# Kernel tuning notes

Hardware: AMD Instinct MI355X
Metric: run time of the kernel (lower is better)

Reference implementation:

```python
import jax, jax.numpy as jnp
import numpy as np

B, S, H, NH, PF, L, V = 8, 1024, 1024, 16, 4096, 6, 32000
HD = H // NH
STD = 0.02
NEG = -1e10


def setup_inputs() -> dict:
    key = jax.random.key(0)
    ks = jax.random.split(key, 12)
    inp = {
        "src": jax.random.randint(ks[0], (B, S), 0, V),
        "src_mask": jnp.ones((B, 1, 1, S), dtype=bool),
        "tok_emb": jax.random.normal(ks[1], (V, H), jnp.float32) * STD,
        "pos_emb": jax.random.normal(ks[2], (S, H), jnp.float32) * STD,
        "Wq": jax.random.normal(ks[3], (L, H, H), jnp.float32) * STD,
        "bq": jnp.zeros((L, H), jnp.float32),
        "Wk": jax.random.normal(ks[4], (L, H, H), jnp.float32) * STD,
        "bk": jnp.zeros((L, H), jnp.float32),
        "Wv": jax.random.normal(ks[5], (L, H, H), jnp.float32) * STD,
        "bv": jnp.zeros((L, H), jnp.float32),
        "Wo": jax.random.normal(ks[6], (L, H, H), jnp.float32) * STD,
        "bo": jnp.zeros((L, H), jnp.float32),
        "W1": jax.random.normal(ks[7], (L, H, PF), jnp.float32) * STD,
        "b1": jnp.zeros((L, PF), jnp.float32),
        "W2": jax.random.normal(ks[8], (L, PF, H), jnp.float32) * STD,
        "b2": jnp.zeros((L, H), jnp.float32),
        "ln1_g": jnp.ones((L, H), jnp.float32),
        "ln1_b": jnp.zeros((L, H), jnp.float32),
        "ln2_g": jnp.ones((L, H), jnp.float32),
        "ln2_b": jnp.zeros((L, H), jnp.float32),
    }
    return inp


def layer_norm(x, g, b, eps=1e-5):
    m = jnp.mean(x, axis=-1, keepdims=True)
    v = jnp.mean((x - m) ** 2, axis=-1, keepdims=True)
    return (x - m) * jax.lax.rsqrt(v + eps) * g + b


def reference(src, src_mask, tok_emb, pos_emb, Wq, bq, Wk, bk, Wv, bv, Wo, bo,
              W1, b1, W2, b2, ln1_g, ln1_b, ln2_g, ln2_b):
    # embedding * sqrt(hid_dim) + positional embedding (dropout = identity at eval)
    x = tok_emb[src] * jnp.sqrt(jnp.float32(H)) + pos_emb[None, :S]
    attn_scale = jnp.sqrt(jnp.float32(HD))
    for l in range(L):
        # multi-head self-attention
        q = (x @ Wq[l] + bq[l]).reshape(B, S, NH, HD).transpose(0, 2, 1, 3)
        k = (x @ Wk[l] + bk[l]).reshape(B, S, NH, HD).transpose(0, 2, 1, 3)
        v = (x @ Wv[l] + bv[l]).reshape(B, S, NH, HD).transpose(0, 2, 1, 3)
        energy = jnp.einsum('bhqd,bhkd->bhqk', q, k) / attn_scale  # [B,NH,S,S]
        energy = jnp.where(src_mask, energy, NEG)
        attn = jax.nn.softmax(energy, axis=-1)
        o = jnp.einsum('bhqk,bhkd->bhqd', attn, v)
        o = o.transpose(0, 2, 1, 3).reshape(B, S, H) @ Wo[l] + bo[l]
        x = layer_norm(x + o, ln1_g[l], ln1_b[l])
        # position-wise feedforward
        f = jax.nn.relu(x @ W1[l] + b1[l]) @ W2[l] + b2[l]
        x = layer_norm(x + f, ln2_g[l], ln2_b[l])
    return x
```

## Files before the change

### kernel.cpp

```cpp
#include <hip/hip_runtime.h>
#include <cstdint>
#include <cstddef>


#define DI __device__ __forceinline__

typedef __attribute__((ext_vector_type(8))) short short8;
typedef __attribute__((ext_vector_type(4))) short s16x4;
typedef __attribute__((ext_vector_type(4))) float f32x4;
typedef __attribute__((ext_vector_type(4))) unsigned u32x4;

static constexpr int H  = 1024;
static constexpr int S  = 1024;
static constexpr int BB = 8;
static constexpr int NH = 16;
static constexpr int PF = 4096;
static constexpr int M  = BB * S;
static constexpr int L  = 6;

DI short f2bf(float f) {
  unsigned u = __builtin_bit_cast(unsigned, f);
  u += 0x7fffu + ((u >> 16) & 1u);
  return (short)(u >> 16);
}

DI unsigned packbf(float a, float b) {
  return (__builtin_bit_cast(unsigned, a) >> 16) |
         (__builtin_bit_cast(unsigned, b) & 0xffff0000u);
}

DI void async16(void* lds, const void* g) {
  __builtin_amdgcn_global_load_lds(
      (const __attribute__((address_space(1))) unsigned*)g,
      (__attribute__((address_space(3))) unsigned*)lds, 16, 0, 0);
}

DI f32x4 mfma16(short8 a, short8 b, f32x4 c) {
  return __builtin_amdgcn_mfma_f32_16x16x32_bf16(a, b, c, 0, 0, 0);
}

__global__ __launch_bounds__(256) void embed_kernel(
    const int* __restrict__ src, const float* __restrict__ tok,
    const float* __restrict__ pos, float* __restrict__ xf,
    short* __restrict__ xb) {
  const int row = blockIdx.x;
  const int s = row & (S - 1);
  const int i0 = threadIdx.x << 2;
  const int v = src[row];
  const float4 te = *(const float4*)(tok + (size_t)v * H + i0);
  const float4 pe = *(const float4*)(pos + (size_t)s * H + i0);
  float o[4] = {te.x * 32.f + pe.x, te.y * 32.f + pe.y,
                te.z * 32.f + pe.z, te.w * 32.f + pe.w};
  *(float4*)(xf + (size_t)row * H + i0) = make_float4(o[0], o[1], o[2], o[3]);
  s16x4 pk;
  pk[0] = f2bf(o[0]); pk[1] = f2bf(o[1]); pk[2] = f2bf(o[2]); pk[3] = f2bf(o[3]);
  *(s16x4*)(xb + (size_t)row * H + i0) = pk;
}

__global__ __launch_bounds__(256) void wconv_layer(
    const float* __restrict__ Wq, const float* __restrict__ Wk,
    const float* __restrict__ Wv, const float* __restrict__ Wo,
    const float* __restrict__ W1, const float* __restrict__ W2,
    const float* __restrict__ bq, const float* __restrict__ bk,
    const float* __restrict__ bv, short* __restrict__ tq,
    short* __restrict__ tk, short* __restrict__ tv, short* __restrict__ to,
    short* __restrict__ t1, short* __restrict__ t2, float* __restrict__ bqkv) {
  const int id = blockIdx.x;
  if (id >= 3072) {
    const int i = (id - 3072) * 256 + threadIdx.x;
    bqkv[i] = (i < 1024) ? bq[i] : (i < 2048) ? bk[i - 1024] : bv[i - 2048];
    return;
  }
  const float* W; short* Wt; int K, N, lb;
  if (id < 256)       { W = Wq; Wt = tq; K = 1024; N = 1024; lb = id; }
  else if (id < 512)  { W = Wk; Wt = tk; K = 1024; N = 1024; lb = id - 256; }
  else if (id < 768)  { W = Wv; Wt = tv; K = 1024; N = 1024; lb = id - 512; }
  else if (id < 1024) { W = Wo; Wt = to; K = 1024; N = 1024; lb = id - 768; }
  else if (id < 2048) { W = W1; Wt = t1; K = 1024; N = 4096; lb = id - 1024; }
  else                { W = W2; Wt = t2; K = 4096; N = 1024; lb = id - 2048; }
  __shared__ float tile[64][65];
  const int ntn = N >> 6;
  const int k0 = (lb / ntn) << 6;
  const int n0 = (lb % ntn) << 6;
  const int r4 = threadIdx.x >> 6, cc = threadIdx.x & 63;
#pragma unroll
  for (int i = 0; i < 16; i++) {
    const int r = (i << 2) + r4;
    tile[r][cc] = W[(size_t)(k0 + r) * N + n0 + cc];
  }
  __syncthreads();
#pragma unroll
  for (int i = 0; i < 16; i++) {
    const int n = (i << 2) + r4;
    Wt[(size_t)(n0 + n) * K + k0 + cc] = f2bf(tile[cc][n]);
  }
}

template <int EPI>
__global__ __launch_bounds__(512, 2) void gemmT(
    const short* __restrict__ A, const short* __restrict__ Bt,
    const float* __restrict__ bias, void* __restrict__ out0,
    short* __restrict__ outK, short* __restrict__ outV,
    const int nbn, const int outN, const int K) {
  extern __shared__ char lds[];
  constexpr int BUF = 49152;
  const int tid = threadIdx.x;
  const int w = tid >> 6, lane = tid & 63;
  const int g = lane >> 4, ci = lane & 15;
  const int wm = w >> 1, wn = w & 1;

  const int bid = (int)blockIdx.x;
  const int xcd = bid & 7, ii = bid >> 3;
  const int bm = ((xcd & 3) << 3) | (ii & 7);
  const int bn = (xcd >> 2) * (nbn >> 1) + (ii >> 3);
  const int brow = bm << 8;
  const int bcol = bn << 7;

  const int srow = tid >> 3;
  const int schk = ((tid & 7) ^ (srow & 7)) << 3;
  const short* aS[4];
#pragma unroll
  for (int j = 0; j < 4; j++)
    aS[j] = A + (size_t)(brow + srow + j * 64) * K + schk;
  const short* bS[2];
#pragma unroll
  for (int j = 0; j < 2; j++)
    bS[j] = Bt + (size_t)(bcol + srow + j * 64) * K + schk;

  auto stA = [&](int t2, int j) {
    async16(lds + (t2 % 3) * BUF + (tid + j * 512) * 16, aS[j] + (t2 << 6));
  };
  auto stB = [&](int t2, int j) {
    async16(lds + (t2 % 3) * BUF + 32768 + (tid + j * 512) * 16,
            bS[j] + (t2 << 6));
  };

  int aoff[2], boff[2];
#pragma unroll
  for (int ks = 0; ks < 2; ks++) {
    const int chk = ((ks * 4 + g) ^ (ci & 7)) << 4;
    aoff[ks] = (wm * 64 + ci) * 128 + chk;
    boff[ks] = 32768 + (wn * 64 + ci) * 128 + chk;
  }

  f32x4 acc[4][4];
#pragma unroll
  for (int a = 0; a < 4; a++)
#pragma unroll
    for (int b = 0; b < 4; b++) acc[a][b] = f32x4{0.f, 0.f, 0.f, 0.f};

  stA(0, 0); stA(0, 1); stB(0, 0); stA(0, 2); stA(0, 3); stB(0, 1);
  stA(1, 0); stA(1, 1); stB(1, 0); stA(1, 2); stA(1, 3); stB(1, 1);
  asm volatile("s_waitcnt vmcnt(6)" ::: "memory");
  __builtin_amdgcn_sched_barrier(0);
  __builtin_amdgcn_s_barrier();

  const int nt = K >> 6;
  for (int t = 0; t < nt; t++) {
    const char* cb = lds + (t % 3) * BUF;
    const bool pf = (t + 2 < nt);
    short8 afr[4], bfr[4];
#pragma unroll
    for (int mi = 0; mi < 4; mi++)
      afr[mi] = *(const short8*)(cb + aoff[0] + mi * 2048);
#pragma unroll
    for (int nj = 0; nj < 4; nj++)
      bfr[nj] = *(const short8*)(cb + boff[0] + nj * 2048);
    if (pf) { stA(t + 2, 0); stA(t + 2, 1); stB(t + 2, 0); }
    __builtin_amdgcn_s_barrier();
    asm volatile("s_waitcnt lgkmcnt(0)" ::: "memory");
    __builtin_amdgcn_sched_barrier(0);
    __builtin_amdgcn_s_setprio(1);
#pragma unroll
    for (int mi = 0; mi < 4; mi++)
#pragma unroll
      for (int nj = 0; nj < 4; nj++)
        acc[mi][nj] = mfma16(afr[mi], bfr[nj], acc[mi][nj]);
    __builtin_amdgcn_s_setprio(0);
    __builtin_amdgcn_s_barrier();
#pragma unroll
    for (int mi = 0; mi < 4; mi++)
      afr[mi] = *(const short8*)(cb + aoff[1] + mi * 2048);
#pragma unroll
    for (int nj = 0; nj < 4; nj++)
      bfr[nj] = *(const short8*)(cb + boff[1] + nj * 2048);
    if (pf) { stA(t + 2, 2); stA(t + 2, 3); stB(t + 2, 1); }
    __builtin_amdgcn_s_barrier();
    asm volatile("s_waitcnt lgkmcnt(0)" ::: "memory");
    __builtin_amdgcn_sched_barrier(0);
    __builtin_amdgcn_s_setprio(1);
#pragma unroll
    for (int mi = 0; mi < 4; mi++)
#pragma unroll
      for (int nj = 0; nj < 4; nj++)
        acc[mi][nj] = mfma16(afr[mi], bfr[nj], acc[mi][nj]);
    __builtin_amdgcn_s_setprio(0);
    if (pf) asm volatile("s_waitcnt vmcnt(6)" ::: "memory");
    else    asm volatile("s_waitcnt vmcnt(0)" ::: "memory");
    __builtin_amdgcn_sched_barrier(0);
    __builtin_amdgcn_s_barrier();
  }

  const bool vpath = (EPI == 4) && (bcol >= 2048);
  if (!vpath) {
    short* oq; const short* dummy; (void)dummy;
    int bc = bcol;
    if constexpr (EPI == 4) {
      oq = (bcol >> 10) ? outK : (short*)out0;
      bc = bcol & 1023;
    }
    float bv[4];
#pragma unroll
    for (int nj = 0; nj < 4; nj++)
      bv[nj] = bias[bcol + wn * 64 + nj * 16 + ci];
#pragma unroll
    for (int mi = 0; mi < 4; mi++) {
#pragma unroll
      for (int r = 0; r < 4; r++) {
        const int row = brow + wm * 64 + mi * 16 + (g << 2) + r;
#pragma unroll
        for (int nj = 0; nj < 4; nj++) {
          const int col = bc + wn * 64 + nj * 16 + ci;
          float vv = acc[mi][nj][r] + bv[nj];
          if constexpr (EPI == 1) vv = fmaxf(vv, 0.f);
          if constexpr (EPI == 2) {
            ((float*)out0)[(size_t)row * outN + col] = vv;
          } else if constexpr (EPI == 4) {
            oq[(size_t)row * outN + col] = f2bf(vv);
          } else {
            ((short*)out0)[(size_t)row * outN + col] = f2bf(vv);
          }
        }
      }
    }
  } else {
    __syncthreads();
    short* tb = (short*)lds;
#pragma unroll
    for (int nj = 0; nj < 4; nj++) {
      const int d = wn * 64 + nj * 16 + ci;
      const float bv = bias[bcol + d];
#pragma unroll
      for (int mi = 0; mi < 4; mi++) {
        const int s = wm * 64 + mi * 16 + (g << 2);
        s16x4 pk;
#pragma unroll
        for (int r = 0; r < 4; r++) pk[r] = f2bf(acc[mi][nj][r] + bv);
        *(s16x4*)(tb + d * 264 + s) = pk;
      }
    }
    __syncthreads();
    const int b = brow >> 10, s0 = brow & (S - 1), d0 = bcol & 1023;
#pragma unroll
    for (int rr = 0; rr < 8; rr++) {
      const int idx = tid + rr * 512;
      const int d = idx >> 5, sc = idx & 31;
      const short8 v = *(const short8*)(tb + d * 264 + sc * 8);
      *(short8*)(outV + ((size_t)b * H + d0 + d) * S + s0 + sc * 8) = v;
    }
  }
}

__global__ __launch_bounds__(256) void attn_kernel(
    const short* __restrict__ q, const short* __restrict__ k,
    const short* __restrict__ vt, short* __restrict__ ao) {
  __shared__ short lsk[2][4096];
  __shared__ short lsv[2][4096];
  const int tid = threadIdx.x;
  const int w = tid >> 6, lane = tid & 63;
  const int g = lane >> 4, ci = lane & 15;
  const int bid = ((int)blockIdx.x & 7) * 256 + ((int)blockIdx.x >> 3);
  const int qt = bid & 15;
  const int bh = bid >> 4;
  const int b = bh >> 4, h = bh & 15;
  const int hbase = h << 6;

  const int r8 = lane >> 3, c8 = lane & 7;
  const int cs = c8 ^ r8;
  const short* kbase = k + ((size_t)b * S) * H + hbase;
  const short* vbase = vt + ((size_t)b * H + hbase) * S;

  const size_t qrow = (size_t)b * S + (qt << 6) + (w << 4) + ci;
  short8 qf[2];
#pragma unroll
  for (int ks = 0; ks < 2; ks++)
    qf[ks] = *(const short8*)(q + qrow * H + hbase + ks * 32 + (g << 3));

  const int swz = ci & 7;
  int koff[2], voff[2][2];
#pragma unroll
  for (int ks = 0; ks < 2; ks++) {
    koff[ks] = ci * 128 + (((4 * ks + g) ^ swz) << 4);
#pragma unroll
    for (int pc = 0; pc < 2; pc++)
      voff[ks][pc] =
          ci * 128 + (((4 * ks + 2 * pc + (g >> 1)) ^ swz) << 4) + ((g & 1) << 3);
  }

#pragma unroll
  for (int t = 0; t < 2; t++) {
    const int row = (w << 3) + t * 32 + r8;
    async16(&lsk[0][t * 2048 + (w << 9)], kbase + (size_t)row * H + cs * 8);
    async16(&lsv[0][t * 2048 + (w << 9)], vbase + (size_t)row * S + cs * 8);
  }
  __syncthreads();

  const f32x4 zero = {0.f, 0.f, 0.f, 0.f};
  f32x4 of[4];
#pragma unroll
  for (int nf = 0; nf < 4; nf++) of[nf] = zero;
  float mrun = -INFINITY, lsum = 0.f;

#pragma unroll 2
  for (int kt = 0; kt < 16; kt++) {
    const int cur = kt & 1;
    if (kt < 15) {
      const int kr1 = (kt + 1) << 6;
#pragma unroll
      for (int t = 0; t < 2; t++) {
        const int row = (w << 3) + t * 32 + r8;
        async16(&lsk[cur ^ 1][t * 2048 + (w << 9)],
                kbase + (size_t)(kr1 + row) * H + cs * 8);
        async16(&lsv[cur ^ 1][t * 2048 + (w << 9)],
                vbase + (size_t)row * S + kr1 + cs * 8);
      }
    }
    const char* kb = (const char*)lsk[cur];
    const char* vb = (const char*)lsv[cur];

    f32x4 st[4];
#pragma unroll
    for (int mf = 0; mf < 4; mf++) st[mf] = zero;
#pragma unroll
    for (int ks = 0; ks < 2; ks++)
#pragma unroll
      for (int mf = 0; mf < 4; mf++) {
        const short8 kf = *(const short8*)(kb + koff[ks] + mf * 2048);
        st[mf] = mfma16(kf, qf[ks], st[mf]);
      }

    float tmax = -INFINITY;
#pragma unroll
    for (int mf = 0; mf < 4; mf++)
#pragma unroll
      for (int r = 0; r < 4; r++) tmax = fmaxf(tmax, st[mf][r]);
    tmax = fmaxf(tmax, __shfl_xor(tmax, 16));
    tmax = fmaxf(tmax, __shfl_xor(tmax, 32));
    const float mnew = fmaxf(mrun, tmax * 0.125f);
    const float alpha = __expf(mrun - mnew);
    float rs = 0.f;
    float p[4][4];
#pragma unroll
    for (int mf = 0; mf < 4; mf++)
#pragma unroll
      for (int r = 0; r < 4; r++) {
        p[mf][r] = __expf(__builtin_fmaf(st[mf][r], 0.125f, -mnew));
        rs += p[mf][r];
      }
    rs += __shfl_xor(rs, 16);
    rs += __shfl_xor(rs, 32);
    lsum = lsum * alpha + rs;
    mrun = mnew;

    unsigned pk[4][2];
#pragma unroll
    for (int mf = 0; mf < 4; mf++) {
      pk[mf][0] = packbf(p[mf][0], p[mf][1]);
      pk[mf][1] = packbf(p[mf][2], p[mf][3]);
    }
#pragma unroll
    for (int nf = 0; nf < 4; nf++)
#pragma unroll
      for (int r = 0; r < 4; r++) of[nf][r] *= alpha;

#pragma unroll
    for (int ks = 0; ks < 2; ks++) {
      u32x4 uu;
      uu[0] = pk[2 * ks][0];
      uu[1] = pk[2 * ks][1];
      uu[2] = pk[2 * ks + 1][0];
      uu[3] = pk[2 * ks + 1][1];
      const short8 pfrag = __builtin_bit_cast(short8, uu);
#pragma unroll
      for (int nf = 0; nf < 4; nf++) {
        union { short8 v8; s16x4 h[2]; } vv;
        vv.h[0] = *(const s16x4*)(vb + voff[ks][0] + nf * 2048);
        vv.h[1] = *(const s16x4*)(vb + voff[ks][1] + nf * 2048);
        of[nf] = mfma16(vv.v8, pfrag, of[nf]);
      }
    }
    __syncthreads();
  }

  const float inv = 1.f / lsum;
#pragma unroll
  for (int nf = 0; nf < 4; nf++) {
    s16x4 o4;
#pragma unroll
    for (int r = 0; r < 4; r++) o4[r] = f2bf(of[nf][r] * inv);
    *(s16x4*)(ao + qrow * H + hbase + (nf << 4) + (g << 2)) = o4;
  }
}

__global__ __launch_bounds__(256) void ln_kernel(
    const float* __restrict__ x, const float* __restrict__ t,
    const float* __restrict__ gm, const float* __restrict__ bt,
    float* __restrict__ yf, short* __restrict__ yb) {
  const int row = blockIdx.x;
  const int i0 = threadIdx.x << 2;
  const size_t base = (size_t)row * H + i0;
  const float4 a = *(const float4*)(x + base);
  const float4 bb = *(const float4*)(t + base);
  float v[4] = {a.x + bb.x, a.y + bb.y, a.z + bb.z, a.w + bb.w};
  float s = v[0] + v[1] + v[2] + v[3];
  float qq = v[0] * v[0] + v[1] * v[1] + v[2] * v[2] + v[3] * v[3];
#pragma unroll
  for (int off = 32; off; off >>= 1) {
    s += __shfl_down(s, off);
    qq += __shfl_down(qq, off);
  }
  __shared__ float red[8];
  const int w = threadIdx.x >> 6, lane = threadIdx.x & 63;
  if (lane == 0) { red[w] = s; red[4 + w] = qq; }
  __syncthreads();
  s = red[0] + red[1] + red[2] + red[3];
  qq = red[4] + red[5] + red[6] + red[7];
  const float mean = s * (1.f / H);
  float var = qq * (1.f / H) - mean * mean;
  var = fmaxf(var, 0.f);
  const float rstd = rsqrtf(var + 1e-5f);
  const float4 gv = *(const float4*)(gm + i0);
  const float4 bv = *(const float4*)(bt + i0);
  float y[4] = {(v[0] - mean) * rstd * gv.x + bv.x,
                (v[1] - mean) * rstd * gv.y + bv.y,
                (v[2] - mean) * rstd * gv.z + bv.z,
                (v[3] - mean) * rstd * gv.w + bv.w};
  *(float4*)(yf + base) = make_float4(y[0], y[1], y[2], y[3]);
  s16x4 pk;
  pk[0] = f2bf(y[0]); pk[1] = f2bf(y[1]); pk[2] = f2bf(y[2]); pk[3] = f2bf(y[3]);
  *(s16x4*)(yb + base) = pk;
}

extern "C" void kernel_launch(void* const* d_in, const int* in_sizes, int n_in,
                              void* d_out, int out_size, void* d_ws, size_t ws_size,
                              hipStream_t stream) {
  const int* src = (const int*)d_in[0];
  const float* tok = (const float*)d_in[2];
  const float* pos = (const float*)d_in[3];
  const float* Wq = (const float*)d_in[4];
  const float* bq = (const float*)d_in[5];
  const float* Wk = (const float*)d_in[6];
  const float* bk = (const float*)d_in[7];
  const float* Wv = (const float*)d_in[8];
  const float* bv = (const float*)d_in[9];
  const float* Wo = (const float*)d_in[10];
  const float* bo = (const float*)d_in[11];
  const float* W1 = (const float*)d_in[12];
  const float* b1 = (const float*)d_in[13];
  const float* W2 = (const float*)d_in[14];
  const float* b2 = (const float*)d_in[15];
  const float* g1 = (const float*)d_in[16];
  const float* be1 = (const float*)d_in[17];
  const float* g2 = (const float*)d_in[18];
  const float* be2 = (const float*)d_in[19];

  hipFuncSetAttribute(reinterpret_cast<const void*>(gemmT<1>),
                      hipFuncAttributeMaxDynamicSharedMemorySize, 147456);
  hipFuncSetAttribute(reinterpret_cast<const void*>(gemmT<2>),
                      hipFuncAttributeMaxDynamicSharedMemorySize, 147456);
  hipFuncSetAttribute(reinterpret_cast<const void*>(gemmT<4>),
                      hipFuncAttributeMaxDynamicSharedMemorySize, 147456);

  char* p = (char*)d_ws;
  auto take = [&](size_t bytes) {
    char* r = p;
    p += (bytes + 255) & ~(size_t)255;
    return r;
  };
  float* xf    = (float*)take((size_t)M * H * 4);
  short* xb    = (short*)take((size_t)M * H * 2);
  float* tmp   = (float*)take((size_t)M * H * 4);
  short* qb    = (short*)take((size_t)M * H * 2);
  short* kbuf  = (short*)take((size_t)M * H * 2);
  short* vtb   = (short*)take((size_t)M * H * 2);
  short* aob   = (short*)take((size_t)M * H * 2);
  short* fb    = (short*)take((size_t)M * PF * 2);
  short* wtqkv = (short*)take((size_t)3 * H * H * 2);
  short* wto   = (short*)take((size_t)H * H * 2);
  short* wt1   = (short*)take((size_t)H * PF * 2);
  short* wt2   = (short*)take((size_t)H * PF * 2);
  float* bqkv  = (float*)take((size_t)3 * H * 4);

  embed_kernel<<<M, 256, 0, stream>>>(src, tok, pos, xf, xb);

  for (int l = 0; l < L; l++) {
    wconv_layer<<<3084, 256, 0, stream>>>(
        Wq + (size_t)l * H * H, Wk + (size_t)l * H * H, Wv + (size_t)l * H * H,
        Wo + (size_t)l * H * H, W1 + (size_t)l * H * PF, W2 + (size_t)l * PF * H,
        bq + (size_t)l * H, bk + (size_t)l * H, bv + (size_t)l * H,
        wtqkv, wtqkv + (size_t)H * H, wtqkv + (size_t)2 * H * H,
        wto, wt1, wt2, bqkv);

    gemmT<4><<<768, 512, 147456, stream>>>(xb, wtqkv, bqkv, qb, kbuf, vtb,
                                           24, H, H);
    attn_kernel<<<BB * NH * (S / 64), 256, 0, stream>>>(qb, kbuf, vtb, aob);
    gemmT<2><<<256, 512, 147456, stream>>>(aob, wto, bo + (size_t)l * H, tmp,
                                           nullptr, nullptr, 8, H, H);
    ln_kernel<<<M, 256, 0, stream>>>(xf, tmp, g1 + (size_t)l * H,
                                     be1 + (size_t)l * H, xf, xb);
    gemmT<1><<<1024, 512, 147456, stream>>>(xb, wt1, b1 + (size_t)l * PF, fb,
                                            nullptr, nullptr, 32, PF, H);
    gemmT<2><<<256, 512, 147456, stream>>>(fb, wt2, b2 + (size_t)l * H, tmp,
                                           nullptr, nullptr, 8, H, PF);
    float* yf = (l == L - 1) ? (float*)d_out : xf;
    ln_kernel<<<M, 256, 0, stream>>>(xf, tmp, g2 + (size_t)l * H,
                                     be2 + (size_t)l * H, yf, xb);
  }
}
```

Before: 2.192 ms.

## Add 256x256-tile GEMM kernel for QKV and FFN1 projections

Introduces gemmQ, a GEMM with 256x256 output tiles (8 waves as 2x4, each computing 128x64) and a double-buffered 64-wide K pipeline split into sub-phases, used for the fused QKV projection and the first FFN layer. Larger tiles raise arithmetic intensity per LDS/global load and halve the grid size. The V-transpose epilogue is done in two halves through LDS. gemmT is reduced to the plain epilogue used only by the N=1024 GEMMs. The cost is higher register pressure from the 32 accumulators per wave and fewer blocks, which may hurt occupancy or tail balance.

```diff
diff --git a/kernel.cpp b/kernel.cpp
--- a/kernel.cpp
+++ b/kernel.cpp
@@ -97,6 +97,161 @@
 }
 
 template <int EPI>
+__global__ __launch_bounds__(512, 2) void gemmQ(
+    const short* __restrict__ A, const short* __restrict__ Bt,
+    const float* __restrict__ bias, void* __restrict__ out0,
+    short* __restrict__ outK, short* __restrict__ outV,
+    const int nbn, const int outN, const int K) {
+  extern __shared__ char lds[];
+  const int tid = threadIdx.x;
+  const int w = tid >> 6, lane = tid & 63;
+  const int g = lane >> 4, ci = lane & 15;
+  const int wm = w >> 2, wn = w & 3;
+
+  const int bid = (int)blockIdx.x;
+  const int xcd = bid & 7, ii = bid >> 3;
+  const int bm = ((xcd & 3) << 3) | (ii & 7);
+  const int bn = (xcd >> 2) * (nbn >> 1) + (ii >> 3);
+  const int brow = bm << 8, bcol = bn << 8;
+
+  const int srow = tid >> 2;
+  const int sch = ((tid & 3) ^ ((tid >> 3) & 3)) << 3;
+  const short* aQ[2];
+  const short* bQ[2];
+#pragma unroll
+  for (int j = 0; j < 2; j++) {
+    aQ[j] = A + (size_t)(brow + srow + j * 128) * K + sch;
+    bQ[j] = Bt + (size_t)(bcol + srow + j * 128) * K + sch;
+  }
+  const int dst0 = tid << 4;
+  auto stg = [&](int nb, int isB, int ks, int ko) {
+    char* base = lds + nb * 65536 + isB * 32768 + ks * 16384;
+    const short* const* src = isB ? bQ : aQ;
+#pragma unroll
+    for (int j = 0; j < 2; j++)
+      async16(base + dst0 + j * 8192, src[j] + ko + ks * 32);
+  };
+
+  const int cswz = (g ^ ((ci >> 1) & 3)) << 4;
+  const int abase = (wm * 128 + ci) * 64 + cswz;
+  const int bbase = 32768 + (wn * 64 + ci) * 64 + cswz;
+
+  f32x4 acc[8][4];
+#pragma unroll
+  for (int a = 0; a < 8; a++)
+#pragma unroll
+    for (int b = 0; b < 4; b++) acc[a][b] = f32x4{0.f, 0.f, 0.f, 0.f};
+
+  stg(0, 0, 0, 0); stg(0, 1, 0, 0); stg(0, 0, 1, 0); stg(0, 1, 1, 0);
+  asm volatile("s_waitcnt vmcnt(4)" ::: "memory");
+  __builtin_amdgcn_sched_barrier(0);
+  __builtin_amdgcn_s_barrier();
+
+  const int nt = K >> 6;
+  for (int t = 0; t < nt; t++) {
+    const char* cb = lds + (t & 1) * 65536;
+    const int nb = (t & 1) ^ 1;
+    const bool pf = (t + 1 < nt);
+    const int ko = (t + 1) << 6;
+    short8 bfr[4];
+#pragma unroll
+    for (int p = 0; p < 4; p++) {
+      const int ks = p >> 1, mh = p & 1;
+      short8 afr[4];
+#pragma unroll
+      for (int fi = 0; fi < 4; fi++)
+        afr[fi] = *(const short8*)(cb + ks * 16384 + abase + mh * 4096 + fi * 1024);
+      if (mh == 0) {
+#pragma unroll
+        for (int fj = 0; fj < 4; fj++)
+          bfr[fj] = *(const short8*)(cb + ks * 16384 + bbase + fj * 1024);
+      }
+      if (pf) stg(nb, p & 1, p >> 1, ko);
+      __builtin_amdgcn_s_barrier();
+      asm volatile("s_waitcnt lgkmcnt(0)" ::: "memory");
+      __builtin_amdgcn_sched_barrier(0);
+      __builtin_amdgcn_s_setprio(1);
+#pragma unroll
+      for (int fi = 0; fi < 4; fi++)
+#pragma unroll
+        for (int fj = 0; fj < 4; fj++)
+          acc[mh * 4 + fi][fj] = mfma16(afr[fi], bfr[fj], acc[mh * 4 + fi][fj]);
+      __builtin_amdgcn_s_setprio(0);
+      if (mh == 1) {
+        if (pf) asm volatile("s_waitcnt vmcnt(4)" ::: "memory");
+        else    asm volatile("s_waitcnt vmcnt(0)" ::: "memory");
+        __builtin_amdgcn_sched_barrier(0);
+      }
+      __builtin_amdgcn_s_barrier();
+    }
+  }
+
+  const bool vpath = (EPI == 4) && (bcol >= 2048);
+  if (!vpath) {
+    short* oq = nullptr;
+    int bc = bcol;
+    if constexpr (EPI == 4) {
+      oq = (bcol < 1024) ? (short*)out0 : outK;
+      bc = bcol & 1023;
+    }
+    float bv[4];
+#pragma unroll
+    for (int fj = 0; fj < 4; fj++)
+      bv[fj] = bias[bcol + wn * 64 + fj * 16 + ci];
+#pragma unroll
+    for (int mi = 0; mi < 8; mi++) {
+#pragma unroll
+      for (int r = 0; r < 4; r++) {
+        const int row = brow + wm * 128 + mi * 16 + (g << 2) + r;
+#pragma unroll
+        for (int fj = 0; fj < 4; fj++) {
+          const int col = bc + wn * 64 + fj * 16 + ci;
+          float vv = acc[mi][fj][r] + bv[fj];
+          if constexpr (EPI == 1) {
+            vv = fmaxf(vv, 0.f);
+            ((short*)out0)[(size_t)row * outN + col] = f2bf(vv);
+          } else {
+            oq[(size_t)row * outN + col] = f2bf(vv);
+          }
+        }
+      }
+    }
+  } else {
+    __syncthreads();
+    short* tb = (short*)lds;
+    const int b = brow >> 10, s0 = brow & (S - 1);
+    const int dG = bcol & 1023;
+#pragma unroll
+    for (int h = 0; h < 2; h++) {
+      if ((wn >> 1) == h) {
+#pragma unroll
+        for (int fj = 0; fj < 4; fj++) {
+          const int d = (wn & 1) * 64 + fj * 16 + ci;
+          const float bv = bias[bcol + wn * 64 + fj * 16 + ci];
+#pragma unroll
+          for (int mi = 0; mi < 8; mi++) {
+            const int s = wm * 128 + mi * 16 + (g << 2);
+            s16x4 pk;
+#pragma unroll
+            for (int r = 0; r < 4; r++) pk[r] = f2bf(acc[mi][fj][r] + bv);
+            *(s16x4*)(tb + d * 264 + s) = pk;
+          }
+        }
+      }
+      __syncthreads();
+#pragma unroll
+      for (int rr = 0; rr < 8; rr++) {
+        const int idx = tid + rr * 512;
+        const int d = idx >> 5, sc = idx & 31;
+        const short8 v = *(const short8*)(tb + d * 264 + sc * 8);
+        *(short8*)(outV + ((size_t)b * H + dG + h * 128 + d) * S + s0 + sc * 8) = v;
+      }
+      __syncthreads();
+    }
+  }
+}
+
+template <int EPI>
 __global__ __launch_bounds__(512, 2) void gemmT(
     const short* __restrict__ A, const short* __restrict__ Bt,
     const float* __restrict__ bias, void* __restrict__ out0,
@@ -201,62 +356,23 @@
     __builtin_amdgcn_s_barrier();
   }
 
-  const bool vpath = (EPI == 4) && (bcol >= 2048);
-  if (!vpath) {
-    short* oq; const short* dummy; (void)dummy;
-    int bc = bcol;
-    if constexpr (EPI == 4) {
-      oq = (bcol >> 10) ? outK : (short*)out0;
-      bc = bcol & 1023;
-    }
-    float bv[4];
-#pragma unroll
-    for (int nj = 0; nj < 4; nj++)
-      bv[nj] = bias[bcol + wn * 64 + nj * 16 + ci];
-#pragma unroll
-    for (int mi = 0; mi < 4; mi++) {
-#pragma unroll
-      for (int r = 0; r < 4; r++) {
-        const int row = brow + wm * 64 + mi * 16 + (g << 2) + r;
-#pragma unroll
-        for (int nj = 0; nj < 4; nj++) {
-          const int col = bc + wn * 64 + nj * 16 + ci;
-          float vv = acc[mi][nj][r] + bv[nj];
-          if constexpr (EPI == 1) vv = fmaxf(vv, 0.f);
-          if constexpr (EPI == 2) {
-            ((float*)out0)[(size_t)row * outN + col] = vv;
-          } else if constexpr (EPI == 4) {
-            oq[(size_t)row * outN + col] = f2bf(vv);
-          } else {
-            ((short*)out0)[(size_t)row * outN + col] = f2bf(vv);
-          }
-        }
-      }
-    }
-  } else {
-    __syncthreads();
-    short* tb = (short*)lds;
-#pragma unroll
-    for (int nj = 0; nj < 4; nj++) {
-      const int d = wn * 64 + nj * 16 + ci;
-      const float bv = bias[bcol + d];
-#pragma unroll
-      for (int mi = 0; mi < 4; mi++) {
-        const int s = wm * 64 + mi * 16 + (g << 2);
-        s16x4 pk;
-#pragma unroll
-        for (int r = 0; r < 4; r++) pk[r] = f2bf(acc[mi][nj][r] + bv);
-        *(s16x4*)(tb + d * 264 + s) = pk;
-      }
-    }
-    __syncthreads();
-    const int b = brow >> 10, s0 = brow & (S - 1), d0 = bcol & 1023;
-#pragma unroll
-    for (int rr = 0; rr < 8; rr++) {
-      const int idx = tid + rr * 512;
-      const int d = idx >> 5, sc = idx & 31;
-      const short8 v = *(const short8*)(tb + d * 264 + sc * 8);
-      *(short8*)(outV + ((size_t)b * H + d0 + d) * S + s0 + sc * 8) = v;
+  float bv[4];
+#pragma unroll
+  for (int nj = 0; nj < 4; nj++)
+    bv[nj] = bias[bcol + wn * 64 + nj * 16 + ci];
+#pragma unroll
+  for (int mi = 0; mi < 4; mi++) {
+#pragma unroll
+    for (int r = 0; r < 4; r++) {
+      const int row = brow + wm * 64 + mi * 16 + (g << 2) + r;
+#pragma unroll
+      for (int nj = 0; nj < 4; nj++) {
+        const int col = bcol + wn * 64 + nj * 16 + ci;
+        float vv = acc[mi][nj][r] + bv[nj];
+        if constexpr (EPI == 1) vv = fmaxf(vv, 0.f);
+        if constexpr (EPI == 2) ((float*)out0)[(size_t)row * outN + col] = vv;
+        else ((short*)out0)[(size_t)row * outN + col] = f2bf(vv);
+      }
     }
   }
 }
@@ -464,11 +580,11 @@
   const float* g2 = (const float*)d_in[18];
   const float* be2 = (const float*)d_in[19];
 
-  hipFuncSetAttribute(reinterpret_cast<const void*>(gemmT<1>),
-                      hipFuncAttributeMaxDynamicSharedMemorySize, 147456);
+  hipFuncSetAttribute(reinterpret_cast<const void*>(gemmQ<1>),
+                      hipFuncAttributeMaxDynamicSharedMemorySize, 131072);
+  hipFuncSetAttribute(reinterpret_cast<const void*>(gemmQ<4>),
+                      hipFuncAttributeMaxDynamicSharedMemorySize, 131072);
   hipFuncSetAttribute(reinterpret_cast<const void*>(gemmT<2>),
-                      hipFuncAttributeMaxDynamicSharedMemorySize, 147456);
-  hipFuncSetAttribute(reinterpret_cast<const void*>(gemmT<4>),
                       hipFuncAttributeMaxDynamicSharedMemorySize, 147456);
 
   char* p = (char*)d_ws;
@@ -501,15 +617,15 @@
         wtqkv, wtqkv + (size_t)H * H, wtqkv + (size_t)2 * H * H,
         wto, wt1, wt2, bqkv);
 
-    gemmT<4><<<768, 512, 147456, stream>>>(xb, wtqkv, bqkv, qb, kbuf, vtb,
-                                           24, H, H);
+    gemmQ<4><<<384, 512, 131072, stream>>>(xb, wtqkv, bqkv, qb, kbuf, vtb,
+                                           12, H, H);
     attn_kernel<<<BB * NH * (S / 64), 256, 0, stream>>>(qb, kbuf, vtb, aob);
     gemmT<2><<<256, 512, 147456, stream>>>(aob, wto, bo + (size_t)l * H, tmp,
                                            nullptr, nullptr, 8, H, H);
     ln_kernel<<<M, 256, 0, stream>>>(xf, tmp, g1 + (size_t)l * H,
                                      be1 + (size_t)l * H, xf, xb);
-    gemmT<1><<<1024, 512, 147456, stream>>>(xb, wt1, b1 + (size_t)l * PF, fb,
-                                            nullptr, nullptr, 32, PF, H);
+    gemmQ<1><<<512, 512, 131072, stream>>>(xb, wt1, b1 + (size_t)l * PF, fb,
+                                           nullptr, nullptr, 16, PF, H);
     gemmT<2><<<256, 512, 147456, stream>>>(fb, wt2, b2 + (size_t)l * H, tmp,
                                            nullptr, nullptr, 8, H, PF);
     float* yf = (l == L - 1) ? (float*)d_out : xf;
```

Result: no change. 2.153 ms (-1.8%).
